# Performance work log

Measured on AMD Instinct MI355X. Metric: run time of the kernel, lower is better.

Reference implementation:

```python
import jax, jax.numpy as jnp
import numpy as np

# --- config (matches init_kwargs) ---
E = 32          # n_routed_experts
G = 8           # n_group
TKG = 4         # topk_group
K = 4           # num_experts_per_tok
D = 2048        # hidden_size
H = 1024        # moe_intermediate_size
HS = 4096       # moe_shared_expert_intermediate_size
SCALE = 2.5     # routed_scaling_factor
CAP = 1024


def setup_inputs() -> dict:
    key = jax.random.key(0)
    ks = jax.random.split(key, 6)
    B, S = 2, 2048
    return dict(
        hidden_states=jax.random.normal(ks[0], (B, S, D), jnp.float32),
        gate_w=jax.random.normal(ks[1], (E, D), jnp.float32) * 0.02,
        bias_corr=jnp.zeros((E,), jnp.float32),  # e_score_correction_bias
        up_w=jax.random.normal(ks[2], (E, H, D), jnp.float32) * 0.02,
        down_w=jax.random.normal(ks[3], (E, D, H), jnp.float32) * 0.02,
        shared_up_w=jax.random.normal(ks[4], (HS, D), jnp.float32) * 0.02,
        shared_down_w=jax.random.normal(ks[5], (D, HS), jnp.float32) * 0.02,
    )


def relu2(x):
    r = jnp.maximum(x, 0.0)
    return r * r


def route_tokens(scores, bias_corr):
    # scores: sigmoid(router_logits), [T, E]
    T = scores.shape[0]
    scores_c = scores + bias_corr                                  # for choice
    group_scores = jax.lax.top_k(scores_c.reshape(T, G, E // G), 2)[0].sum(-1)  # [T, G]
    _, group_idx = jax.lax.top_k(group_scores, TKG)                # [T, TKG]
    group_mask = jnp.zeros((T, G), scores.dtype).at[jnp.arange(T)[:, None], group_idx].set(1.0)
    score_mask = jnp.repeat(group_mask, E // G, axis=1)            # [T, E]
    masked = jnp.where(score_mask > 0, scores_c, 0.0)
    _, topk_idx = jax.lax.top_k(masked, K)                         # [T, K]
    topk_w = jnp.take_along_axis(scores, topk_idx, axis=1)         # weights from raw sigmoid scores
    topk_w = topk_w / (topk_w.sum(-1, keepdims=True) + 1e-20)      # norm_topk_prob
    return topk_idx, topk_w * SCALE


def reference(hidden_states, gate_w, bias_corr, up_w, down_w, shared_up_w, shared_down_w):
    B, S, _ = hidden_states.shape
    T = B * S
    flat = hidden_states.reshape(T, D)

    logits = flat @ gate_w.T                                       # [T, E]
    scores = jax.nn.sigmoid(logits)
    topk_idx, topk_w = route_tokens(scores, bias_corr)             # [T, K] each

    # --- capacity-based dispatch (equivalent to per-expert gather + index_add combine) ---
    e_flat = topk_idx.reshape(-1)                                  # [T*K]
    oh = jax.nn.one_hot(e_flat, E, dtype=jnp.int32)                # [T*K, E]
    pos = jnp.take_along_axis(jnp.cumsum(oh, axis=0) - 1, e_flat[:, None], axis=1)[:, 0]
    tok = jnp.repeat(jnp.arange(T), K)                             # token idx per assignment
    valid = pos < CAP

    xe = jnp.zeros((E, CAP, D), flat.dtype).at[e_flat, pos].set(flat[tok], mode='drop')
    h = relu2(jnp.einsum('ecd,ehd->ech', xe, up_w))                # [E, CAP, H]
    ye = jnp.einsum('ech,edh->ecd', h, down_w)                     # [E, CAP, D]

    gathered = ye[e_flat, jnp.minimum(pos, CAP - 1)]               # [T*K, D]
    gathered = jnp.where(valid[:, None], gathered, 0.0) * topk_w.reshape(-1)[:, None]
    routed = gathered.reshape(T, K, D).sum(axis=1).reshape(B, S, D)

    shared = relu2(hidden_states @ shared_up_w.T) @ shared_down_w.T
    return routed + shared
```

## Files before the change

kernel.cpp:

```cpp
#include <hip/hip_runtime.h>

#define NE 32
#define NG 8
#define NK 4
#define ND 2048
#define NH 1024
#define NHS 4096
#define CAPE 1024
#define NT 4096

typedef float f32x4 __attribute__((ext_vector_type(4)));
typedef short s16x8 __attribute__((ext_vector_type(8)));

__device__ __forceinline__ short f2bf(float f) {
    return __builtin_bit_cast(short, (__bf16)f);
}
__device__ __forceinline__ float bf2f(short h) {
    return __builtin_bit_cast(float, ((unsigned)(unsigned short)h) << 16);
}

__device__ __forceinline__ void gload_lds16(const void* g, void* l) {
    __builtin_amdgcn_global_load_lds(
        (const __attribute__((address_space(1))) void*)g,
        (__attribute__((address_space(3))) void*)l, 16, 0, 0);
}

__global__ __launch_bounds__(256) void gate_kernel(
    const float* __restrict__ X, const float* __restrict__ Gw,
    const float* __restrict__ bias,
    int* __restrict__ topk_idx, float* __restrict__ topk_w,
    int* __restrict__ cnt)
{
    if (blockIdx.x == 0 && threadIdx.x < NE) cnt[threadIdx.x] = 0;

    const int lane = threadIdx.x & 63;
    const int t = blockIdx.x * 4 + (threadIdx.x >> 6);
    const float* x = X + (size_t)t * ND;

    float xr[32];
#pragma unroll
    for (int i = 0; i < 32; i++) xr[i] = x[lane + i * 64];

    float scores[32];
#pragma unroll
    for (int e = 0; e < 32; e++) {
        const float* w = Gw + (size_t)e * ND;
        float a = 0.f;
#pragma unroll
        for (int i = 0; i < 32; i++) a = fmaf(xr[i], w[lane + i * 64], a);
#pragma unroll
        for (int s = 32; s > 0; s >>= 1) a += __shfl_xor(a, s);
        scores[e] = 1.0f / (1.0f + expf(-a));
    }

    float sc_c[32];
#pragma unroll
    for (int e = 0; e < 32; e++) sc_c[e] = scores[e] + bias[e];

    float gs[8];
#pragma unroll
    for (int g = 0; g < 8; g++) {
        float a = sc_c[4 * g], b = sc_c[4 * g + 1], c = sc_c[4 * g + 2], d = sc_c[4 * g + 3];
        float hi1 = fmaxf(a, b), lo1 = fminf(a, b);
        float hi2 = fmaxf(c, d), lo2 = fminf(c, d);
        float m1 = fmaxf(hi1, hi2);
        float m2 = fmaxf(fminf(hi1, hi2), fmaxf(lo1, lo2));
        gs[g] = m1 + m2;
    }

    unsigned gsel = 0;
#pragma unroll
    for (int it = 0; it < 4; it++) {
        int best = -1; float bv = -1e30f;
#pragma unroll
        for (int g = 0; g < 8; g++) {
            bool avail = !((gsel >> g) & 1);
            if (avail && gs[g] > bv) { bv = gs[g]; best = g; }
        }
        gsel |= 1u << best;
    }

    unsigned esel = 0;
    int idxs[4]; float wts[4];
#pragma unroll
    for (int it = 0; it < 4; it++) {
        int best = -1; float bv = -1e30f, braw = 0.f;
#pragma unroll
        for (int e = 0; e < 32; e++) {
            float mv = ((gsel >> (e >> 2)) & 1) ? sc_c[e] : 0.0f;
            bool avail = !((esel >> e) & 1);
            if (avail && mv > bv) { bv = mv; best = e; braw = scores[e]; }
        }
        esel |= 1u << best;
        idxs[it] = best; wts[it] = braw;
    }

    float s = wts[0] + wts[1] + wts[2] + wts[3] + 1e-20f;
    if (lane == 0) {
#pragma unroll
        for (int k = 0; k < 4; k++) {
            topk_idx[t * 4 + k] = idxs[k];
            topk_w[t * 4 + k] = wts[k] / s * 2.5f;
        }
    }
}

__global__ void dispatch_kernel(const int* __restrict__ topk_idx,
                                int* __restrict__ cnt,
                                int* __restrict__ tok_list,
                                int* __restrict__ pos_list)
{
    int i = blockIdx.x * 256 + threadIdx.x;
    int e = topk_idx[i];
    int t = i >> 2;
    int pos = atomicAdd(&cnt[e], 1);
    pos_list[i] = pos;
    if (pos < CAPE) {
        tok_list[e * CAPE + pos] = t;
    }
}

__global__ __launch_bounds__(256) void cvt_f2bf(const float* __restrict__ in,
                                                short* __restrict__ out, int n8)
{
    int i = blockIdx.x * 256 + threadIdx.x;
    int stride = gridDim.x * 256;
    for (; i < n8; i += stride) {
        const f32x4* p = (const f32x4*)(in + (size_t)i * 8);
        f32x4 a = p[0], b = p[1];
        s16x8 h;
        h[0] = f2bf(a[0]); h[1] = f2bf(a[1]); h[2] = f2bf(a[2]); h[3] = f2bf(a[3]);
        h[4] = f2bf(b[0]); h[5] = f2bf(b[1]); h[6] = f2bf(b[2]); h[7] = f2bf(b[3]);
        *(s16x8*)(out + (size_t)i * 8) = h;
    }
}

__global__ __launch_bounds__(256) void combine_kernel(
    const int* __restrict__ topk_idx, const float* __restrict__ topk_w,
    const int* __restrict__ pos_list,
    const short* __restrict__ Ybuf, float* __restrict__ out)
{
    const int t = blockIdx.x;
    const int d0 = threadIdx.x * 8;

    int e[NK], p[NK]; float w[NK];
#pragma unroll
    for (int k = 0; k < NK; k++) {
        e[k] = topk_idx[t * NK + k];
        p[k] = pos_list[t * NK + k];
        w[k] = topk_w[t * NK + k];
    }

    float* orow = out + (size_t)t * ND + d0;
    f32x4 o0 = *(f32x4*)(orow);
    f32x4 o1 = *(f32x4*)(orow + 4);

#pragma unroll
    for (int k = 0; k < NK; k++) {
        if (p[k] < CAPE) {
            s16x8 y = *(const s16x8*)(Ybuf + ((size_t)e[k] * CAPE + p[k]) * ND + d0);
            o0[0] = fmaf(w[k], bf2f(y[0]), o0[0]);
            o0[1] = fmaf(w[k], bf2f(y[1]), o0[1]);
            o0[2] = fmaf(w[k], bf2f(y[2]), o0[2]);
            o0[3] = fmaf(w[k], bf2f(y[3]), o0[3]);
            o1[0] = fmaf(w[k], bf2f(y[4]), o1[0]);
            o1[1] = fmaf(w[k], bf2f(y[5]), o1[1]);
            o1[2] = fmaf(w[k], bf2f(y[6]), o1[2]);
            o1[3] = fmaf(w[k], bf2f(y[7]), o1[3]);
        }
    }
    *(f32x4*)(orow) = o0;
    *(f32x4*)(orow + 4) = o1;
}

#define GEMM_BODY_SETUP()                                                       \
    __shared__ short As[2][128 * 64];                                           \
    __shared__ short Bs[2][128 * 64];                                           \
    const int tid = threadIdx.x;                                                \
    const int lane = tid & 63;                                                  \
    const int wave = tid >> 6;                                                  \
    const int wr = wave >> 1, wc = wave & 1;                                    \
    const int srow = tid >> 3;                                                  \
    const int pA = tid & 7;                                                     \
    const int gcolA = (pA ^ (srow & 7)) * 8;                                    \
    const int brow = tid >> 4;                                                  \
    const int lc = tid & 15;                                                    \
    const int r16 = lane & 15;                                                  \
    const int physbase = ((lane >> 4) ^ (lane & 7)) * 8;                        \
    int offA[4], offB[4];                                                       \
    _Pragma("unroll")                                                           \
    for (int m = 0; m < 4; m++) offA[m] = (wr * 64 + m * 16 + r16) * 64 + physbase; \
    _Pragma("unroll")                                                           \
    for (int n = 0; n < 4; n++) offB[n] = (wc * 64 + n * 16 + r16) * 64 + physbase;

#define GEMM_ITER(T, PAR, CONSUME, FILL)                                        \
    {                                                                           \
        __builtin_amdgcn_s_barrier();                                           \
        __builtin_amdgcn_sched_barrier(0);                                      \
        BLOAD((T) + 3, FILL);                                                   \
        const short* At = As[PAR];                                              \
        const short* Bt = Bs[PAR];                                              \
        s16x8 af[4], bf[4];                                                     \
        _Pragma("unroll")                                                       \
        for (int m = 0; m < 4; m++) af[m] = *(const s16x8*)(At + offA[m]);      \
        _Pragma("unroll")                                                       \
        for (int n = 0; n < 4; n++) bf[n] = *(const s16x8*)(Bt + offB[n]);      \
        asm volatile("s_waitcnt lgkmcnt(0)" ::: "memory");                      \
        __builtin_amdgcn_sched_barrier(0);                                      \
        __builtin_amdgcn_s_setprio(1);                                          \
        _Pragma("unroll")                                                       \
        for (int m = 0; m < 4; m++)                                             \
            _Pragma("unroll")                                                   \
            for (int n = 0; n < 4; n++)                                         \
                acc[m][n] = __builtin_amdgcn_mfma_f32_16x16x32_bf16(            \
                    af[m], bf[n], acc[m][n], 0, 0, 0);                          \
        __builtin_amdgcn_s_setprio(0);                                          \
        s16x8 ag[4], bg[4];                                                     \
        _Pragma("unroll")                                                       \
        for (int m = 0; m < 4; m++) ag[m] = *(const s16x8*)(At + (offA[m] ^ 32)); \
        _Pragma("unroll")                                                       \
        for (int n = 0; n < 4; n++) bg[n] = *(const s16x8*)(Bt + (offB[n] ^ 32)); \
        asm volatile("s_waitcnt lgkmcnt(0)" ::: "memory");                      \
        __builtin_amdgcn_sched_barrier(0);                                      \
        __builtin_amdgcn_s_barrier();         \
        __builtin_amdgcn_sched_barrier(0);                                      \
        STAGE_A((T) + 2, PAR);                                                  \
        asm volatile("s_waitcnt vmcnt(12)" ::: "memory");  \
        __builtin_amdgcn_sched_barrier(0);                                      \
        BWRITE(CONSUME, PAR);                            \
        __builtin_amdgcn_s_setprio(1);                                          \
        _Pragma("unroll")                                                       \
        for (int m = 0; m < 4; m++)                                             \
            _Pragma("unroll")                                                   \
            for (int n = 0; n < 4; n++)                                         \
                acc[m][n] = __builtin_amdgcn_mfma_f32_16x16x32_bf16(            \
                    ag[m], bg[n], acc[m][n], 0, 0, 0);                          \
        __builtin_amdgcn_s_setprio(0);                                          \
        asm volatile("s_waitcnt lgkmcnt(0)" ::: "memory");                      \
        __builtin_amdgcn_sched_barrier(0);                                      \
    }

#define GEMM_PROLOGUE()                                                         \
    STAGE_A(0, 0); STAGE_A(1, 1);                                               \
    BLOAD(0, brE); BLOAD(1, brO);                                               \
    asm volatile("s_waitcnt vmcnt(8)" ::: "memory");                            \
    __builtin_amdgcn_sched_barrier(0);                                          \
    BWRITE(brE, 0);                                                             \
    asm volatile("s_waitcnt vmcnt(0)" ::: "memory");                            \
    __builtin_amdgcn_sched_barrier(0);                                          \
    BWRITE(brO, 1);                                                             \
    BLOAD(2, brE);                                                              \
    asm volatile("s_waitcnt lgkmcnt(0)" ::: "memory");                          \
    __builtin_amdgcn_sched_barrier(0);

__global__ __launch_bounds__(256, 2) void fused_up(
    const short* __restrict__ Xbf, const float* __restrict__ up_w,
    const float* __restrict__ sup,
    const int* __restrict__ cnt, const int* __restrict__ tok_list,
    short* __restrict__ Hbuf, short* __restrict__ Sbuf)
{
    constexpr int K = ND;
    constexpr int NTILES = K / 64;

    const int bid = blockIdx.x;
    const bool routed = bid < 2048;
    int e = 0, m0, n0, mcnt = 0;
    const float* Bb;
    if (routed) {
        e = bid >> 6;
        m0 = ((bid >> 3) & 7) * 128;
        n0 = (bid & 7) * 128;
        mcnt = min(cnt[e], CAPE);
        if (m0 >= mcnt) return;
        Bb = up_w + (size_t)e * NH * ND;
    } else {
        int lin = bid - 2048;
        m0 = (lin >> 5) * 128;
        n0 = (lin & 31) * 128;
        Bb = sup;
    }

    GEMM_BODY_SETUP();

    const short* asrc[4];
    int dstA[4];
#pragma unroll
    for (int o = 0; o < 4; o++) {
        int r = o * 32 + srow;
        int arow;
        if (routed) {
            int gr = min(m0 + r, mcnt - 1);
            arow = tok_list[e * CAPE + gr];
        } else {
            arow = m0 + r;
        }
        asrc[o] = Xbf + (size_t)arow * ND + gcolA;
        dstA[o] = o * 2048 + wave * 512;
    }

    const float* bsrc[8];
    int bdst[8];
#pragma unroll
    for (int o = 0; o < 8; o++) {
        int r = o * 16 + brow;
        bsrc[o] = Bb + (size_t)(n0 + r) * K + lc * 4;
        int ks = lc >> 1;
        bdst[o] = r * 64 + ((ks ^ (r & 7)) * 8) + (lc & 1) * 4;
    }

    auto STAGE_A = [&](int tt, int par) {
        const int ko = (tt < NTILES ? tt : NTILES - 1) * 64;
        short* Ad = As[par];
#pragma unroll
        for (int o = 0; o < 4; o++) gload_lds16(asrc[o] + ko, Ad + dstA[o]);
    };
    auto BLOAD = [&](int tt, f32x4* regs) {
        const int ko = (tt < NTILES ? tt : NTILES - 1) * 64;
#pragma unroll
        for (int o = 0; o < 8; o++) regs[o] = *(const f32x4*)(bsrc[o] + ko);
    };
    auto BWRITE = [&](const f32x4* regs, int par) {
        short* Bd = Bs[par];
#pragma unroll
        for (int o = 0; o < 8; o++) {
            short4 h;
            h.x = f2bf(regs[o][0]); h.y = f2bf(regs[o][1]);
            h.z = f2bf(regs[o][2]); h.w = f2bf(regs[o][3]);
            *(short4*)(Bd + bdst[o]) = h;
        }
    };

    f32x4 acc[4][4] = {};
    f32x4 brE[8], brO[8];

    GEMM_PROLOGUE();
    for (int t = 0; t < NTILES; t += 2) {
        GEMM_ITER(t,     0, brE, brO);
        GEMM_ITER(t + 1, 1, brO, brE);
    }

    const int r0 = (lane >> 4) * 4;
    const int cc = lane & 15;
#pragma unroll
    for (int i = 0; i < 4; i++)
#pragma unroll
        for (int j = 0; j < 4; j++)
#pragma unroll
            for (int v = 0; v < 4; v++) {
                int row = wr * 64 + i * 16 + r0 + v;
                int col = wc * 64 + j * 16 + cc;
                float val = acc[i][j][v];
                float r = fmaxf(val, 0.f);
                val = r * r;
                if (routed)
                    Hbuf[((size_t)e * CAPE + m0 + row) * NH + (n0 + col)] = f2bf(val);
                else
                    Sbuf[(size_t)(m0 + row) * NHS + (n0 + col)] = f2bf(val);
            }
}

__global__ __launch_bounds__(256, 2) void fused_dn(
    const short* __restrict__ Hbuf, const short* __restrict__ Sbuf,
    const float* __restrict__ dn_w, const float* __restrict__ sdn,
    const int* __restrict__ cnt, const int* __restrict__ tok_list,
    short* __restrict__ Ybuf, float* __restrict__ out)
{
    const int bid = blockIdx.x;
    const bool routed = bid < 4096;
    int e = 0, m0, n0, mcnt = 0;
    int K;
    const short* Abase;
    const float* Bb;
    if (routed) {
        e = bid >> 7;
        m0 = ((bid >> 4) & 7) * 128;
        n0 = (bid & 15) * 128;
        mcnt = min(cnt[e], CAPE);
        if (m0 >= mcnt) return;
        K = NH;
        Abase = Hbuf + (size_t)e * CAPE * NH;
        Bb = dn_w + (size_t)e * ND * NH;
    } else {
        int lin = bid - 4096;
        m0 = (lin >> 4) * 128;
        n0 = (lin & 15) * 128;
        K = NHS;
        Abase = Sbuf;
        Bb = sdn;
    }
    const int NTILES = K / 64;

    GEMM_BODY_SETUP();

    const short* asrc[4];
    int dstA[4];
#pragma unroll
    for (int o = 0; o < 4; o++) {
        int r = o * 32 + srow;
        int arow = routed ? min(m0 + r, mcnt - 1) : (m0 + r);
        asrc[o] = Abase + (size_t)arow * K + gcolA;
        dstA[o] = o * 2048 + wave * 512;
    }

    const float* bsrc[8];
    int bdst[8];
#pragma unroll
    for (int o = 0; o < 8; o++) {
        int r = o * 16 + brow;
        bsrc[o] = Bb + (size_t)(n0 + r) * K + lc * 4;
        int ks = lc >> 1;
        bdst[o] = r * 64 + ((ks ^ (r & 7)) * 8) + (lc & 1) * 4;
    }

    auto STAGE_A = [&](int tt, int par) {
        const int ko = (tt < NTILES ? tt : NTILES - 1) * 64;
        short* Ad = As[par];
#pragma unroll
        for (int o = 0; o < 4; o++) gload_lds16(asrc[o] + ko, Ad + dstA[o]);
    };
    auto BLOAD = [&](int tt, f32x4* regs) {
        const int ko = (tt < NTILES ? tt : NTILES - 1) * 64;
#pragma unroll
        for (int o = 0; o < 8; o++) regs[o] = *(const f32x4*)(bsrc[o] + ko);
    };
    auto BWRITE = [&](const f32x4* regs, int par) {
        short* Bd = Bs[par];
#pragma unroll
        for (int o = 0; o < 8; o++) {
            short4 h;
            h.x = f2bf(regs[o][0]); h.y = f2bf(regs[o][1]);
            h.z = f2bf(regs[o][2]); h.w = f2bf(regs[o][3]);
            *(short4*)(Bd + bdst[o]) = h;
        }
    };

    f32x4 acc[4][4] = {};
    f32x4 brE[8], brO[8];

    GEMM_PROLOGUE();
    for (int t = 0; t < NTILES; t += 2) {
        GEMM_ITER(t,     0, brE, brO);
        GEMM_ITER(t + 1, 1, brO, brE);
    }

    const int r0 = (lane >> 4) * 4;
    const int cc = lane & 15;
    if (routed) {
#pragma unroll
        for (int i = 0; i < 4; i++)
#pragma unroll
            for (int v = 0; v < 4; v++) {
                int row = wr * 64 + i * 16 + r0 + v;
                int grow = m0 + row;
                if (grow < mcnt) {
#pragma unroll
                    for (int j = 0; j < 4; j++) {
                        int col = wc * 64 + j * 16 + cc;
                        Ybuf[((size_t)e * CAPE + grow) * ND + (n0 + col)] = f2bf(acc[i][j][v]);
                    }
                }
            }
    } else {
#pragma unroll
        for (int i = 0; i < 4; i++)
#pragma unroll
            for (int j = 0; j < 4; j++)
#pragma unroll
                for (int v = 0; v < 4; v++) {
                    int row = wr * 64 + i * 16 + r0 + v;
                    int col = wc * 64 + j * 16 + cc;
                    out[(size_t)(m0 + row) * ND + (n0 + col)] = acc[i][j][v];
                }
    }
}

extern "C" void kernel_launch(void* const* d_in, const int* in_sizes, int n_in,
                              void* d_out, int out_size, void* d_ws, size_t ws_size,
                              hipStream_t stream) {
    const float* X    = (const float*)d_in[0];
    const float* Gw   = (const float*)d_in[1];
    const float* bias = (const float*)d_in[2];
    const float* up_w = (const float*)d_in[3];
    const float* dn_w = (const float*)d_in[4];
    const float* sup  = (const float*)d_in[5];
    const float* sdn  = (const float*)d_in[6];
    float* out = (float*)d_out;

    char* ws = (char*)d_ws;
    size_t off = 0;
    auto alloc = [&](size_t bytes) -> void* {
        off = (off + 255) & ~(size_t)255;
        void* p = ws + off;
        off += bytes;
        return p;
    };
    int*   cnt      = (int*)  alloc(NE * 4);
    int*   topk_idx = (int*)  alloc((size_t)NT * NK * 4);
    float* topk_w   = (float*)alloc((size_t)NT * NK * 4);
    int*   pos_list = (int*)  alloc((size_t)NT * NK * 4);
    int*   tok_list = (int*)  alloc((size_t)NE * CAPE * 4);
    short* Hbuf     = (short*)alloc((size_t)NE * CAPE * NH * 2);
    short* Sbuf     = (short*)alloc((size_t)NT * NHS * 2);
    short* Xbf      = (short*)alloc((size_t)NT * ND * 2);
    short* Ybuf     = (short*)alloc((size_t)NE * CAPE * ND * 2);

    gate_kernel<<<dim3(NT / 4), dim3(256), 0, stream>>>(X, Gw, bias, topk_idx, topk_w, cnt);
    dispatch_kernel<<<dim3(NT * NK / 256), dim3(256), 0, stream>>>(
        topk_idx, cnt, tok_list, pos_list);

    cvt_f2bf<<<dim3(1024), dim3(256), 0, stream>>>(X, Xbf, NT * ND / 8);

    fused_up<<<dim3(2048 + 1024), dim3(256), 0, stream>>>(
        Xbf, up_w, sup, cnt, tok_list, Hbuf, Sbuf);
    fused_dn<<<dim3(4096 + 512), dim3(256), 0, stream>>>(
        Hbuf, Sbuf, dn_w, sdn, cnt, tok_list, Ybuf, out);
    combine_kernel<<<dim3(NT), dim3(256), 0, stream>>>(
        topk_idx, topk_w, pos_list, Ybuf, out);
}
```

Measured before the change: 638.9 us.

## Split 128x128 GEMM tile across 8 waves instead of 4

Both fused up and down GEMM kernels now launch 512 threads per block. The 128x128 output tile is split into 2x4 wave sub-tiles of 64x32 instead of 2x2 sub-tiles of 64x64, and each thread's A/B staging loads are halved. The vmcnt wait thresholds are adjusted to match. The aim is more waves per CU to hide memory latency, with fewer accumulator registers per thread and launch bounds of (512,4). The trade-off is more LDS fragment reads per MFMA, since each A fragment is reused across only two B fragments, plus barrier cost across 8 waves.

```diff
diff --git a/kernel.cpp b/kernel.cpp
--- a/kernel.cpp
+++ b/kernel.cpp
@@ -179,19 +179,19 @@
     const int tid = threadIdx.x;                                                \
     const int lane = tid & 63;                                                  \
     const int wave = tid >> 6;                                                  \
-    const int wr = wave >> 1, wc = wave & 1;                                    \
-    const int srow = tid >> 3;                                                  \
+    const int wrM = wave >> 2, wrN = wave & 3;                                  \
+    const int srow = tid >> 3;                  \
     const int pA = tid & 7;                                                     \
     const int gcolA = (pA ^ (srow & 7)) * 8;                                    \
-    const int brow = tid >> 4;                                                  \
-    const int lc = tid & 15;                                                    \
+    const int brow = tid >> 2;                       \
+    const int bq = tid & 3;                   \
     const int r16 = lane & 15;                                                  \
     const int physbase = ((lane >> 4) ^ (lane & 7)) * 8;                        \
-    int offA[4], offB[4];                                                       \
+    int offA[4], offB[2];                                                       \
     _Pragma("unroll")                                                           \
-    for (int m = 0; m < 4; m++) offA[m] = (wr * 64 + m * 16 + r16) * 64 + physbase; \
+    for (int m = 0; m < 4; m++) offA[m] = (wrM * 64 + m * 16 + r16) * 64 + physbase; \
     _Pragma("unroll")                                                           \
-    for (int n = 0; n < 4; n++) offB[n] = (wc * 64 + n * 16 + r16) * 64 + physbase;
+    for (int n = 0; n < 2; n++) offB[n] = (wrN * 32 + n * 16 + r16) * 64 + physbase;
 
 #define GEMM_ITER(T, PAR, CONSUME, FILL)                                        \
     {                                                                           \
@@ -200,39 +200,39 @@
         BLOAD((T) + 3, FILL);                                                   \
         const short* At = As[PAR];                                              \
         const short* Bt = Bs[PAR];                                              \
-        s16x8 af[4], bf[4];                                                     \
+        s16x8 af[4], bf[2];                                                     \
         _Pragma("unroll")                                                       \
         for (int m = 0; m < 4; m++) af[m] = *(const s16x8*)(At + offA[m]);      \
         _Pragma("unroll")                                                       \
-        for (int n = 0; n < 4; n++) bf[n] = *(const s16x8*)(Bt + offB[n]);      \
+        for (int n = 0; n < 2; n++) bf[n] = *(const s16x8*)(Bt + offB[n]);      \
         asm volatile("s_waitcnt lgkmcnt(0)" ::: "memory");                      \
         __builtin_amdgcn_sched_barrier(0);                                      \
         __builtin_amdgcn_s_setprio(1);                                          \
         _Pragma("unroll")                                                       \
         for (int m = 0; m < 4; m++)                                             \
             _Pragma("unroll")                                                   \
-            for (int n = 0; n < 4; n++)                                         \
+            for (int n = 0; n < 2; n++)                                         \
                 acc[m][n] = __builtin_amdgcn_mfma_f32_16x16x32_bf16(            \
                     af[m], bf[n], acc[m][n], 0, 0, 0);                          \
         __builtin_amdgcn_s_setprio(0);                                          \
-        s16x8 ag[4], bg[4];                                                     \
+        s16x8 ag[4], bg[2];                                                     \
         _Pragma("unroll")                                                       \
         for (int m = 0; m < 4; m++) ag[m] = *(const s16x8*)(At + (offA[m] ^ 32)); \
         _Pragma("unroll")                                                       \
-        for (int n = 0; n < 4; n++) bg[n] = *(const s16x8*)(Bt + (offB[n] ^ 32)); \
+        for (int n = 0; n < 2; n++) bg[n] = *(const s16x8*)(Bt + (offB[n] ^ 32)); \
         asm volatile("s_waitcnt lgkmcnt(0)" ::: "memory");                      \
         __builtin_amdgcn_sched_barrier(0);                                      \
         __builtin_amdgcn_s_barrier();         \
         __builtin_amdgcn_sched_barrier(0);                                      \
         STAGE_A((T) + 2, PAR);                                                  \
-        asm volatile("s_waitcnt vmcnt(12)" ::: "memory");  \
+        asm volatile("s_waitcnt vmcnt(6)" ::: "memory");  \
         __builtin_amdgcn_sched_barrier(0);                                      \
         BWRITE(CONSUME, PAR);                            \
         __builtin_amdgcn_s_setprio(1);                                          \
         _Pragma("unroll")                                                       \
         for (int m = 0; m < 4; m++)                                             \
             _Pragma("unroll")                                                   \
-            for (int n = 0; n < 4; n++)                                         \
+            for (int n = 0; n < 2; n++)                                         \
                 acc[m][n] = __builtin_amdgcn_mfma_f32_16x16x32_bf16(            \
                     ag[m], bg[n], acc[m][n], 0, 0, 0);                          \
         __builtin_amdgcn_s_setprio(0);                                          \
@@ -243,17 +243,17 @@
 #define GEMM_PROLOGUE()                                                         \
     STAGE_A(0, 0); STAGE_A(1, 1);                                               \
     BLOAD(0, brE); BLOAD(1, brO);                                               \
-    asm volatile("s_waitcnt vmcnt(8)" ::: "memory");                            \
+    asm volatile("s_waitcnt vmcnt(4)" ::: "memory");           \
     __builtin_amdgcn_sched_barrier(0);                                          \
     BWRITE(brE, 0);                                                             \
-    asm volatile("s_waitcnt vmcnt(0)" ::: "memory");                            \
+    asm volatile("s_waitcnt vmcnt(0)" ::: "memory");                 \
     __builtin_amdgcn_sched_barrier(0);                                          \
     BWRITE(brO, 1);                                                             \
     BLOAD(2, brE);                                                              \
     asm volatile("s_waitcnt lgkmcnt(0)" ::: "memory");                          \
     __builtin_amdgcn_sched_barrier(0);
 
-__global__ __launch_bounds__(256, 2) void fused_up(
+__global__ __launch_bounds__(512, 4) void fused_up(
     const short* __restrict__ Xbf, const float* __restrict__ up_w,
     const float* __restrict__ sup,
     const int* __restrict__ cnt, const int* __restrict__ tok_list,
@@ -282,11 +282,11 @@
 
     GEMM_BODY_SETUP();
 
-    const short* asrc[4];
-    int dstA[4];
-#pragma unroll
-    for (int o = 0; o < 4; o++) {
-        int r = o * 32 + srow;
+    const short* asrc[2];
+    int dstA[2];
+#pragma unroll
+    for (int o = 0; o < 2; o++) {
+        int r = o * 64 + srow;
         int arow;
         if (routed) {
             int gr = min(m0 + r, mcnt - 1);
@@ -295,43 +295,43 @@
             arow = m0 + r;
         }
         asrc[o] = Xbf + (size_t)arow * ND + gcolA;
-        dstA[o] = o * 2048 + wave * 512;
-    }
-
-    const float* bsrc[8];
-    int bdst[8];
-#pragma unroll
-    for (int o = 0; o < 8; o++) {
-        int r = o * 16 + brow;
-        bsrc[o] = Bb + (size_t)(n0 + r) * K + lc * 4;
+        dstA[o] = o * 4096 + wave * 512;
+    }
+
+    const float* bsrc[4];
+    int bdst[4];
+#pragma unroll
+    for (int i = 0; i < 4; i++) {
+        int lc = bq * 4 + i;
+        bsrc[i] = Bb + (size_t)(n0 + brow) * K + lc * 4;
         int ks = lc >> 1;
-        bdst[o] = r * 64 + ((ks ^ (r & 7)) * 8) + (lc & 1) * 4;
+        bdst[i] = brow * 64 + ((ks ^ (brow & 7)) * 8) + (lc & 1) * 4;
     }
 
     auto STAGE_A = [&](int tt, int par) {
         const int ko = (tt < NTILES ? tt : NTILES - 1) * 64;
         short* Ad = As[par];
 #pragma unroll
-        for (int o = 0; o < 4; o++) gload_lds16(asrc[o] + ko, Ad + dstA[o]);
+        for (int o = 0; o < 2; o++) gload_lds16(asrc[o] + ko, Ad + dstA[o]);
     };
     auto BLOAD = [&](int tt, f32x4* regs) {
         const int ko = (tt < NTILES ? tt : NTILES - 1) * 64;
 #pragma unroll
-        for (int o = 0; o < 8; o++) regs[o] = *(const f32x4*)(bsrc[o] + ko);
+        for (int i = 0; i < 4; i++) regs[i] = *(const f32x4*)(bsrc[i] + ko);
     };
     auto BWRITE = [&](const f32x4* regs, int par) {
         short* Bd = Bs[par];
 #pragma unroll
-        for (int o = 0; o < 8; o++) {
+        for (int i = 0; i < 4; i++) {
             short4 h;
-            h.x = f2bf(regs[o][0]); h.y = f2bf(regs[o][1]);
-            h.z = f2bf(regs[o][2]); h.w = f2bf(regs[o][3]);
-            *(short4*)(Bd + bdst[o]) = h;
-        }
-    };
-
-    f32x4 acc[4][4] = {};
-    f32x4 brE[8], brO[8];
+            h.x = f2bf(regs[i][0]); h.y = f2bf(regs[i][1]);
+            h.z = f2bf(regs[i][2]); h.w = f2bf(regs[i][3]);
+            *(short4*)(Bd + bdst[i]) = h;
+        }
+    };
+
+    f32x4 acc[4][2] = {};
+    f32x4 brE[4], brO[4];
 
     GEMM_PROLOGUE();
     for (int t = 0; t < NTILES; t += 2) {
@@ -344,11 +344,11 @@
 #pragma unroll
     for (int i = 0; i < 4; i++)
 #pragma unroll
-        for (int j = 0; j < 4; j++)
+        for (int j = 0; j < 2; j++)
 #pragma unroll
             for (int v = 0; v < 4; v++) {
-                int row = wr * 64 + i * 16 + r0 + v;
-                int col = wc * 64 + j * 16 + cc;
+                int row = wrM * 64 + i * 16 + r0 + v;
+                int col = wrN * 32 + j * 16 + cc;
                 float val = acc[i][j][v];
                 float r = fmaxf(val, 0.f);
                 val = r * r;
@@ -359,7 +359,7 @@
             }
 }
 
-__global__ __launch_bounds__(256, 2) void fused_dn(
+__global__ __launch_bounds__(512, 4) void fused_dn(
     const short* __restrict__ Hbuf, const short* __restrict__ Sbuf,
     const float* __restrict__ dn_w, const float* __restrict__ sdn,
     const int* __restrict__ cnt, const int* __restrict__ tok_list,
@@ -392,50 +392,50 @@
 
     GEMM_BODY_SETUP();
 
-    const short* asrc[4];
-    int dstA[4];
-#pragma unroll
-    for (int o = 0; o < 4; o++) {
-        int r = o * 32 + srow;
+    const short* asrc[2];
+    int dstA[2];
+#pragma unroll
+    for (int o = 0; o < 2; o++) {
+        int r = o * 64 + srow;
         int arow = routed ? min(m0 + r, mcnt - 1) : (m0 + r);
         asrc[o] = Abase + (size_t)arow * K + gcolA;
-        dstA[o] = o * 2048 + wave * 512;
-    }
-
-    const float* bsrc[8];
-    int bdst[8];
-#pragma unroll
-    for (int o = 0; o < 8; o++) {
-        int r = o * 16 + brow;
-        bsrc[o] = Bb + (size_t)(n0 + r) * K + lc * 4;
+        dstA[o] = o * 4096 + wave * 512;
+    }
+
+    const float* bsrc[4];
+    int bdst[4];
+#pragma unroll
+    for (int i = 0; i < 4; i++) {
+        int lc = bq * 4 + i;
+        bsrc[i] = Bb + (size_t)(n0 + brow) * K + lc * 4;
         int ks = lc >> 1;
-        bdst[o] = r * 64 + ((ks ^ (r & 7)) * 8) + (lc & 1) * 4;
+        bdst[i] = brow * 64 + ((ks ^ (brow & 7)) * 8) + (lc & 1) * 4;
     }
 
     auto STAGE_A = [&](int tt, int par) {
         const int ko = (tt < NTILES ? tt : NTILES - 1) * 64;
         short* Ad = As[par];
 #pragma unroll
-        for (int o = 0; o < 4; o++) gload_lds16(asrc[o] + ko, Ad + dstA[o]);
+        for (int o = 0; o < 2; o++) gload_lds16(asrc[o] + ko, Ad + dstA[o]);
     };
     auto BLOAD = [&](int tt, f32x4* regs) {
         const int ko = (tt < NTILES ? tt : NTILES - 1) * 64;
 #pragma unroll
-        for (int o = 0; o < 8; o++) regs[o] = *(const f32x4*)(bsrc[o] + ko);
+        for (int i = 0; i < 4; i++) regs[i] = *(const f32x4*)(bsrc[i] + ko);
     };
     auto BWRITE = [&](const f32x4* regs, int par) {
         short* Bd = Bs[par];
 #pragma unroll
-        for (int o = 0; o < 8; o++) {
+        for (int i = 0; i < 4; i++) {
             short4 h;
-            h.x = f2bf(regs[o][0]); h.y = f2bf(regs[o][1]);
-            h.z = f2bf(regs[o][2]); h.w = f2bf(regs[o][3]);
-            *(short4*)(Bd + bdst[o]) = h;
-        }
-    };
-
-    f32x4 acc[4][4] = {};
-    f32x4 brE[8], brO[8];
+            h.x = f2bf(regs[i][0]); h.y = f2bf(regs[i][1]);
+            h.z = f2bf(regs[i][2]); h.w = f2bf(regs[i][3]);
+            *(short4*)(Bd + bdst[i]) = h;
+        }
+    };
+
+    f32x4 acc[4][2] = {};
+    f32x4 brE[4], brO[4];
 
     GEMM_PROLOGUE();
     for (int t = 0; t < NTILES; t += 2) {
@@ -450,12 +450,12 @@
         for (int i = 0; i < 4; i++)
 #pragma unroll
             for (int v = 0; v < 4; v++) {
-                int row = wr * 64 + i * 16 + r0 + v;
+                int row = wrM * 64 + i * 16 + r0 + v;
                 int grow = m0 + row;
                 if (grow < mcnt) {
 #pragma unroll
-                    for (int j = 0; j < 4; j++) {
-                        int col = wc * 64 + j * 16 + cc;
+                    for (int j = 0; j < 2; j++) {
+                        int col = wrN * 32 + j * 16 + cc;
                         Ybuf[((size_t)e * CAPE + grow) * ND + (n0 + col)] = f2bf(acc[i][j][v]);
                     }
                 }
@@ -464,11 +464,11 @@
 #pragma unroll
         for (int i = 0; i < 4; i++)
 #pragma unroll
-            for (int j = 0; j < 4; j++)
+            for (int j = 0; j < 2; j++)
 #pragma unroll
                 for (int v = 0; v < 4; v++) {
-                    int row = wr * 64 + i * 16 + r0 + v;
-                    int col = wc * 64 + j * 16 + cc;
+                    int row = wrM * 64 + i * 16 + r0 + v;
+                    int col = wrN * 32 + j * 16 + cc;
                     out[(size_t)(m0 + row) * ND + (n0 + col)] = acc[i][j][v];
                 }
     }
@@ -510,9 +510,9 @@
 
     cvt_f2bf<<<dim3(1024), dim3(256), 0, stream>>>(X, Xbf, NT * ND / 8);
 
-    fused_up<<<dim3(2048 + 1024), dim3(256), 0, stream>>>(
+    fused_up<<<dim3(2048 + 1024), dim3(512), 0, stream>>>(
         Xbf, up_w, sup, cnt, tok_list, Hbuf, Sbuf);
-    fused_dn<<<dim3(4096 + 512), dim3(256), 0, stream>>>(
+    fused_dn<<<dim3(4096 + 512), dim3(512), 0, stream>>>(
         Hbuf, Sbuf, dn_w, sdn, cnt, tok_list, Ybuf, out);
     combine_kernel<<<dim3(NT), dim3(256), 0, stream>>>(
         topk_idx, topk_w, pos_list, Ybuf, out);
```

After: 710.7 us. +11.2%, slower.

## Pre-convert down-proj weights to bf16 in extra up-kernel blocks, simplify dn pipeline

Applied to the files above, without the earlier changes.

Extra blocks appended to the up-projection launch convert the routed and shared down-projection weights from fp32 to bf16, so the conversion can overlap with the up GEMM tail. The down kernel then streams both A and B tiles straight into LDS with direct global-to-LDS loads, replacing the register load, convert and LDS write path for B. This halves the down-GEMM weight bytes read and removes the in-loop conversion. In exchange it adds a full extra pass that reads fp32 and writes bf16 for about 80M weights on every call, plus workspace for the bf16 copies.

```diff
diff --git a/kernel.cpp b/kernel.cpp
--- a/kernel.cpp
+++ b/kernel.cpp
@@ -222,12 +222,12 @@
         for (int n = 0; n < 4; n++) bg[n] = *(const s16x8*)(Bt + (offB[n] ^ 32)); \
         asm volatile("s_waitcnt lgkmcnt(0)" ::: "memory");                      \
         __builtin_amdgcn_sched_barrier(0);                                      \
-        __builtin_amdgcn_s_barrier();         \
+        __builtin_amdgcn_s_barrier();                                           \
         __builtin_amdgcn_sched_barrier(0);                                      \
         STAGE_A((T) + 2, PAR);                                                  \
-        asm volatile("s_waitcnt vmcnt(12)" ::: "memory");  \
+        asm volatile("s_waitcnt vmcnt(12)" ::: "memory");                       \
         __builtin_amdgcn_sched_barrier(0);                                      \
-        BWRITE(CONSUME, PAR);                            \
+        BWRITE(CONSUME, PAR);                                                   \
         __builtin_amdgcn_s_setprio(1);                                          \
         _Pragma("unroll")                                                       \
         for (int m = 0; m < 4; m++)                                             \
@@ -253,16 +253,44 @@
     asm volatile("s_waitcnt lgkmcnt(0)" ::: "memory");                          \
     __builtin_amdgcn_sched_barrier(0);
 
+#define NCVT 2176
 __global__ __launch_bounds__(256, 2) void fused_up(
     const short* __restrict__ Xbf, const float* __restrict__ up_w,
     const float* __restrict__ sup,
+    const float* __restrict__ dn_w, const float* __restrict__ sdn,
     const int* __restrict__ cnt, const int* __restrict__ tok_list,
-    short* __restrict__ Hbuf, short* __restrict__ Sbuf)
+    short* __restrict__ Hbuf, short* __restrict__ Sbuf,
+    short* __restrict__ dn_bf, short* __restrict__ sdn_bf)
 {
     constexpr int K = ND;
     constexpr int NTILES = K / 64;
 
     const int bid = blockIdx.x;
+    if (bid >= 3072) {
+        const int cid = bid - 3072;
+        int i = cid * 256 + threadIdx.x;
+        const int stride = NCVT * 256;
+        const int n8dn = NE * ND * NH / 8;
+        for (int v = i; v < n8dn; v += stride) {
+            const f32x4* p = (const f32x4*)(dn_w + (size_t)v * 8);
+            f32x4 a = p[0], b = p[1];
+            s16x8 h;
+            h[0] = f2bf(a[0]); h[1] = f2bf(a[1]); h[2] = f2bf(a[2]); h[3] = f2bf(a[3]);
+            h[4] = f2bf(b[0]); h[5] = f2bf(b[1]); h[6] = f2bf(b[2]); h[7] = f2bf(b[3]);
+            *(s16x8*)(dn_bf + (size_t)v * 8) = h;
+        }
+        const int n8sd = ND * NHS / 8;
+        for (int v = i; v < n8sd; v += stride) {
+            const f32x4* p = (const f32x4*)(sdn + (size_t)v * 8);
+            f32x4 a = p[0], b = p[1];
+            s16x8 h;
+            h[0] = f2bf(a[0]); h[1] = f2bf(a[1]); h[2] = f2bf(a[2]); h[3] = f2bf(a[3]);
+            h[4] = f2bf(b[0]); h[5] = f2bf(b[1]); h[6] = f2bf(b[2]); h[7] = f2bf(b[3]);
+            *(s16x8*)(sdn_bf + (size_t)v * 8) = h;
+        }
+        return;
+    }
+
     const bool routed = bid < 2048;
     int e = 0, m0, n0, mcnt = 0;
     const float* Bb;
@@ -361,7 +389,7 @@
 
 __global__ __launch_bounds__(256, 2) void fused_dn(
     const short* __restrict__ Hbuf, const short* __restrict__ Sbuf,
-    const float* __restrict__ dn_w, const float* __restrict__ sdn,
+    const short* __restrict__ dn_bf, const short* __restrict__ sdn_bf,
     const int* __restrict__ cnt, const int* __restrict__ tok_list,
     short* __restrict__ Ybuf, float* __restrict__ out)
 {
@@ -370,7 +398,7 @@
     int e = 0, m0, n0, mcnt = 0;
     int K;
     const short* Abase;
-    const float* Bb;
+    const short* Bb;
     if (routed) {
         e = bid >> 7;
         m0 = ((bid >> 4) & 7) * 128;
@@ -379,68 +407,102 @@
         if (m0 >= mcnt) return;
         K = NH;
         Abase = Hbuf + (size_t)e * CAPE * NH;
-        Bb = dn_w + (size_t)e * ND * NH;
+        Bb = dn_bf + (size_t)e * ND * NH;
     } else {
         int lin = bid - 4096;
         m0 = (lin >> 4) * 128;
         n0 = (lin & 15) * 128;
         K = NHS;
         Abase = Sbuf;
-        Bb = sdn;
+        Bb = sdn_bf;
     }
     const int NTILES = K / 64;
 
-    GEMM_BODY_SETUP();
-
+    __shared__ short As[2][128 * 64];
+    __shared__ short Bs[2][128 * 64];
+
+    const int tid = threadIdx.x;
+    const int lane = tid & 63;
+    const int wave = tid >> 6;
+    const int wr = wave >> 1, wc = wave & 1;
+
+    const int srow = tid >> 3;
+    const int p = tid & 7;
+    const int gcol = (p ^ (srow & 7)) * 8;
     const short* asrc[4];
-    int dstA[4];
+    const short* bsrc[4];
+    int dstoff[4];
 #pragma unroll
     for (int o = 0; o < 4; o++) {
         int r = o * 32 + srow;
         int arow = routed ? min(m0 + r, mcnt - 1) : (m0 + r);
-        asrc[o] = Abase + (size_t)arow * K + gcolA;
-        dstA[o] = o * 2048 + wave * 512;
-    }
-
-    const float* bsrc[8];
-    int bdst[8];
-#pragma unroll
-    for (int o = 0; o < 8; o++) {
-        int r = o * 16 + brow;
-        bsrc[o] = Bb + (size_t)(n0 + r) * K + lc * 4;
-        int ks = lc >> 1;
-        bdst[o] = r * 64 + ((ks ^ (r & 7)) * 8) + (lc & 1) * 4;
-    }
-
-    auto STAGE_A = [&](int tt, int par) {
+        asrc[o] = Abase + (size_t)arow * K + gcol;
+        bsrc[o] = Bb + (size_t)(n0 + o * 32 + srow) * K + gcol;
+        dstoff[o] = o * 2048 + wave * 512;
+    }
+
+    auto STAGE = [&](int tt) {
         const int ko = (tt < NTILES ? tt : NTILES - 1) * 64;
-        short* Ad = As[par];
-#pragma unroll
-        for (int o = 0; o < 4; o++) gload_lds16(asrc[o] + ko, Ad + dstA[o]);
+        short* Ad = As[tt & 1];
+        short* Bd = Bs[tt & 1];
+#pragma unroll
+        for (int o = 0; o < 4; o++) gload_lds16(asrc[o] + ko, Ad + dstoff[o]);
+#pragma unroll
+        for (int o = 0; o < 4; o++) gload_lds16(bsrc[o] + ko, Bd + dstoff[o]);
     };
-    auto BLOAD = [&](int tt, f32x4* regs) {
-        const int ko = (tt < NTILES ? tt : NTILES - 1) * 64;
-#pragma unroll
-        for (int o = 0; o < 8; o++) regs[o] = *(const f32x4*)(bsrc[o] + ko);
-    };
-    auto BWRITE = [&](const f32x4* regs, int par) {
-        short* Bd = Bs[par];
-#pragma unroll
-        for (int o = 0; o < 8; o++) {
-            short4 h;
-            h.x = f2bf(regs[o][0]); h.y = f2bf(regs[o][1]);
-            h.z = f2bf(regs[o][2]); h.w = f2bf(regs[o][3]);
-            *(short4*)(Bd + bdst[o]) = h;
-        }
-    };
+
+    const int r16 = lane & 15;
+    const int physbase = ((lane >> 4) ^ (lane & 7)) * 8;
+    int offA[4], offB[4];
+#pragma unroll
+    for (int m = 0; m < 4; m++)
+        offA[m] = (wr * 64 + m * 16 + r16) * 64 + physbase;
+#pragma unroll
+    for (int n = 0; n < 4; n++)
+        offB[n] = (wc * 64 + n * 16 + r16) * 64 + physbase;
 
     f32x4 acc[4][4] = {};
-    f32x4 brE[8], brO[8];
-
-    GEMM_PROLOGUE();
-    for (int t = 0; t < NTILES; t += 2) {
-        GEMM_ITER(t,     0, brE, brO);
-        GEMM_ITER(t + 1, 1, brO, brE);
+
+    STAGE(0);
+    STAGE(1);
+
+    for (int t = 0; t < NTILES; ++t) {
+        const short* At = As[t & 1];
+        const short* Bt = Bs[t & 1];
+        asm volatile("s_waitcnt vmcnt(8)" ::: "memory");
+        __builtin_amdgcn_s_barrier();
+        __builtin_amdgcn_sched_barrier(0);
+        s16x8 af[4], bf[4];
+#pragma unroll
+        for (int m = 0; m < 4; m++) af[m] = *(const s16x8*)(At + offA[m]);
+#pragma unroll
+        for (int n = 0; n < 4; n++) bf[n] = *(const s16x8*)(Bt + offB[n]);
+        asm volatile("s_waitcnt lgkmcnt(0)" ::: "memory");
+        __builtin_amdgcn_sched_barrier(0);
+        __builtin_amdgcn_s_setprio(1);
+#pragma unroll
+        for (int m = 0; m < 4; m++)
+#pragma unroll
+            for (int n = 0; n < 4; n++)
+                acc[m][n] = __builtin_amdgcn_mfma_f32_16x16x32_bf16(af[m], bf[n], acc[m][n], 0, 0, 0);
+        __builtin_amdgcn_s_setprio(0);
+        s16x8 ag[4], bg[4];
+#pragma unroll
+        for (int m = 0; m < 4; m++) ag[m] = *(const s16x8*)(At + (offA[m] ^ 32));
+#pragma unroll
+        for (int n = 0; n < 4; n++) bg[n] = *(const s16x8*)(Bt + (offB[n] ^ 32));
+        asm volatile("s_waitcnt lgkmcnt(0)" ::: "memory");
+        __builtin_amdgcn_sched_barrier(0);
+        __builtin_amdgcn_s_barrier();
+        __builtin_amdgcn_sched_barrier(0);
+        STAGE(t + 2);
+        __builtin_amdgcn_s_setprio(1);
+#pragma unroll
+        for (int m = 0; m < 4; m++)
+#pragma unroll
+            for (int n = 0; n < 4; n++)
+                acc[m][n] = __builtin_amdgcn_mfma_f32_16x16x32_bf16(ag[m], bg[n], acc[m][n], 0, 0, 0);
+        __builtin_amdgcn_s_setprio(0);
     }
 
     const int r0 = (lane >> 4) * 4;
@@ -503,6 +565,8 @@
     short* Sbuf     = (short*)alloc((size_t)NT * NHS * 2);
     short* Xbf      = (short*)alloc((size_t)NT * ND * 2);
     short* Ybuf     = (short*)alloc((size_t)NE * CAPE * ND * 2);
+    short* dn_bf    = (short*)alloc((size_t)NE * ND * NH * 2);
+    short* sdn_bf   = (short*)alloc((size_t)ND * NHS * 2);
 
     gate_kernel<<<dim3(NT / 4), dim3(256), 0, stream>>>(X, Gw, bias, topk_idx, topk_w, cnt);
     dispatch_kernel<<<dim3(NT * NK / 256), dim3(256), 0, stream>>>(
@@ -510,10 +574,10 @@
 
     cvt_f2bf<<<dim3(1024), dim3(256), 0, stream>>>(X, Xbf, NT * ND / 8);
 
-    fused_up<<<dim3(2048 + 1024), dim3(256), 0, stream>>>(
-        Xbf, up_w, sup, cnt, tok_list, Hbuf, Sbuf);
+    fused_up<<<dim3(3072 + NCVT), dim3(256), 0, stream>>>(
+        Xbf, up_w, sup, dn_w, sdn, cnt, tok_list, Hbuf, Sbuf, dn_bf, sdn_bf);
     fused_dn<<<dim3(4096 + 512), dim3(256), 0, stream>>>(
-        Hbuf, Sbuf, dn_w, sdn, cnt, tok_list, Ybuf, out);
+        Hbuf, Sbuf, dn_bf, sdn_bf, cnt, tok_list, Ybuf, out);
     combine_kernel<<<dim3(NT), dim3(256), 0, stream>>>(
         topk_idx, topk_w, pos_list, Ybuf, out);
 }
```

New measurement: 639.6 us. Within noise of the previous version (+0.1%).
